# Performance work log

Hardware: AMD Instinct MI355X
Metric: run time of the kernel (lower is better)

The kernel has to match this reference:

```python
import jax, jax.numpy as jnp
import numpy as np

N_NODES = 20000
D = 512
H = 8
DK = D // H  # 64
L = 2


def _layernorm(x, g, b, eps=1e-5):
    mu = x.mean(-1, keepdims=True)
    var = x.var(-1, keepdims=True)
    return (x - mu) / jnp.sqrt(var + eps) * g + b


def _hgt_layer(h, kw, kb, qw, qb, vw, vb, aw, ab, pri, att_r, msg_r, skip, ln_g, ln_b, src, dst):
    # h: [N, D]
    N = h.shape[0]
    k = (h @ kw.T + kb).reshape(N, H, DK)
    q = (h @ qw.T + qb).reshape(N, H, DK)
    v = (h @ vw.T + vb).reshape(N, H, DK)
    # per-relation bilinear transforms on keys and messages
    k = jnp.einsum('nhi,hij->nhj', k, att_r)
    v = jnp.einsum('nhi,hij->nhj', v, msg_r)
    # per-edge attention scores [E, H]
    t = jnp.einsum('ehd,ehd->eh', k[src], q[dst]) * pri / jnp.sqrt(jnp.float32(DK))
    # edge softmax over incoming edges of each destination node
    mx = jax.ops.segment_max(t, dst, num_segments=N)
    e = jnp.exp(t - mx[dst])
    den = jax.ops.segment_sum(e, dst, num_segments=N)
    att = e / jnp.maximum(den[dst], 1e-9)
    # weighted message aggregation [N, H, DK] -> [N, D]
    msg = v[src] * att[..., None]
    agg = jax.ops.segment_sum(msg, dst, num_segments=N).reshape(N, D)
    trans = jax.nn.gelu(agg) @ aw.T + ab
    alpha = jax.nn.sigmoid(skip)
    out = trans * alpha + h * (1.0 - alpha)
    return _layernorm(out, ln_g, ln_b)


def setup_inputs() -> dict:
    key = jax.random.key(0)
    ks = jax.random.split(key, 16)
    B, E = 8192, 320000
    s = 0.02
    inp = {
        'embeddings': jax.random.normal(ks[0], (B, D), jnp.float32),
        'node_emb': jax.random.normal(ks[1], (N_NODES, D), jnp.float32) * s,
        'adapt_w': jax.random.normal(ks[2], (D, D), jnp.float32) * s,
        'adapt_b': jnp.zeros((D,), jnp.float32),
        'kw': jax.random.normal(ks[3], (L, D, D), jnp.float32) * s,
        'kb': jnp.zeros((L, D), jnp.float32),
        'qw': jax.random.normal(ks[4], (L, D, D), jnp.float32) * s,
        'qb': jnp.zeros((L, D), jnp.float32),
        'vw': jax.random.normal(ks[5], (L, D, D), jnp.float32) * s,
        'vb': jnp.zeros((L, D), jnp.float32),
        'aw': jax.random.normal(ks[6], (L, D, D), jnp.float32) * s,
        'ab': jnp.zeros((L, D), jnp.float32),
        'pri': jnp.ones((L, H), jnp.float32),
        'att_r': jax.random.normal(ks[7], (L, H, DK, DK), jnp.float32) * (1.0 / np.sqrt(DK)),
        'msg_r': jax.random.normal(ks[8], (L, H, DK, DK), jnp.float32) * (1.0 / np.sqrt(DK)),
        'skip': jnp.ones((L,), jnp.float32),
        'ln_g': jnp.ones((L, D), jnp.float32),
        'ln_b': jnp.zeros((L, D), jnp.float32),
        'out_w': jax.random.normal(ks[9], (D, D), jnp.float32) * s,
        'out_b': jnp.zeros((D,), jnp.float32),
        'attn_kernels': jax.random.uniform(ks[10], (D,), jnp.float32),
        'src': jax.random.randint(ks[11], (E,), 0, N_NODES, jnp.int32),
        'dst': jax.random.randint(ks[12], (E,), 0, N_NODES, jnp.int32),
        'n_classes': 10000,
    }
    return inp


def reference(embeddings, node_emb, adapt_w, adapt_b, kw, kb, qw, qb, vw, vb, aw, ab,
              pri, att_r, msg_r, skip, ln_g, ln_b, out_w, out_b, attn_kernels,
              src, dst, n_classes):
    # Hgt encoder over the label graph (single ntype '_N')
    h = jax.nn.gelu(node_emb @ adapt_w.T + adapt_b)
    for l in range(L):
        h = _hgt_layer(h, kw[l], kb[l], qw[l], qb[l], vw[l], vb[l], aw[l], ab[l],
                       pri[l], att_r[l], msg_r[l], skip[l], ln_g[l], ln_b[l], src, dst)
    cls_emb = h @ out_w.T + out_b          # [N, D]
    cls_emb = cls_emb[:n_classes]          # [C, D]  (dropout is identity in eval)
    # logits[b,c] = sum_d embeddings[b,d] * attn_kernels[d] * cls_emb[c,d]
    logits = (embeddings * attn_kernels) @ cls_emb.T
    return logits
```

## Files before the change

kernel.cpp:

```cpp
#include <hip/hip_runtime.h>
#include <hip/hip_bf16.h>

#define D 512
#define H 8
#define NLAYER 2

typedef __attribute__((ext_vector_type(8))) short short8;
typedef __attribute__((ext_vector_type(4))) short short4v;
typedef __attribute__((ext_vector_type(4))) float f32x4;

__device__ __forceinline__ float gelu_f(float x) {
    float x3 = x * x * x;
    return 0.5f * x * (1.0f + tanhf(0.7978845608028654f * (x + 0.044715f * x3)));
}

__device__ __forceinline__ unsigned short f2b(float x) {
    unsigned u = __float_as_uint(x);
    u += 0x7FFF + ((u >> 16) & 1);
    return (unsigned short)(u >> 16);
}
__device__ __forceinline__ float b2f(unsigned short u) {
    return __uint_as_float(((unsigned)u) << 16);
}

template <int POSTG, int OUTMODE>
__global__ __launch_bounds__(256) void gemm_bf(
    const short* __restrict__ A, const short* __restrict__ B,
    const float* __restrict__ bias, float* __restrict__ Cf,
    short* __restrict__ Cb, int M, int N, int K) {
    __shared__ __align__(16) short As[128 * 40];
    __shared__ __align__(16) short Bs[128 * 40];
    const unsigned gx = gridDim.x, gy = gridDim.y;
    const unsigned nwg = gx * gy;
    const unsigned orig = blockIdx.y * gx + blockIdx.x;
    const unsigned q = nwg >> 3, r = nwg & 7;
    const unsigned xcd = orig & 7, sidx = orig >> 3;
    const unsigned swz = (xcd < r ? xcd * (q + 1) : r * (q + 1) + (xcd - r) * q) + sidx;
    const unsigned CH = 8;
    const unsigned chunk = swz / (CH * gx);
    const unsigned rem = swz - chunk * (CH * gx);
    const unsigned nr = min(CH, gy - chunk * CH);
    const unsigned col = rem / nr;
    const unsigned rowin = rem - col * nr;
    const int bm = (int)(chunk * CH + rowin) * 128;
    const int bn = (int)col * 128;

    const int tid = threadIdx.x;
    const int lane = tid & 63;
    const int wave = tid >> 6;
    const int wm = (wave >> 1) * 64, wn = (wave & 1) * 64;
    const int lr16 = lane & 15;
    const int lk8 = (lane >> 4) * 8;

    const int srow = tid >> 1;
    const int skb = (tid & 1) * 16;
    const int arow = min(bm + srow, M - 1);
    const int brow = min(bn + srow, N - 1);
    const short* Ap = A + (size_t)arow * K + skb;
    const short* Bp = B + (size_t)brow * K + skb;

    f32x4 acc[4][4];
#pragma unroll
    for (int i = 0; i < 4; ++i)
#pragma unroll
        for (int j = 0; j < 4; ++j) acc[i][j] = (f32x4){0.f, 0.f, 0.f, 0.f};

    short8 ra0, ra1, rb0, rb1;
    auto load_ab = [&](int k0) {
        ra0 = *(const short8*)(Ap + k0);
        ra1 = *(const short8*)(Ap + k0 + 8);
        rb0 = *(const short8*)(Bp + k0);
        rb1 = *(const short8*)(Bp + k0 + 8);
    };

    load_ab(0);
    for (int k0 = 0; k0 < K; k0 += 32) {
        __syncthreads();
        *(short8*)&As[srow * 40 + skb]     = ra0;
        *(short8*)&As[srow * 40 + skb + 8] = ra1;
        *(short8*)&Bs[srow * 40 + skb]     = rb0;
        *(short8*)&Bs[srow * 40 + skb + 8] = rb1;
        __syncthreads();
        if (k0 + 32 < K) load_ab(k0 + 32);

        short8 af[4], bfr[4];
#pragma unroll
        for (int mi = 0; mi < 4; ++mi)
            af[mi] = *(const short8*)&As[(wm + mi * 16 + lr16) * 40 + lk8];
#pragma unroll
        for (int ni = 0; ni < 4; ++ni)
            bfr[ni] = *(const short8*)&Bs[(wn + ni * 16 + lr16) * 40 + lk8];
#pragma unroll
        for (int mi = 0; mi < 4; ++mi)
#pragma unroll
            for (int ni = 0; ni < 4; ++ni)
                acc[mi][ni] = __builtin_amdgcn_mfma_f32_16x16x32_bf16(
                    af[mi], bfr[ni], acc[mi][ni], 0, 0, 0);
    }

#pragma unroll
    for (int mi = 0; mi < 4; ++mi) {
        int row0 = bm + wm + mi * 16 + (lane >> 4) * 4;
#pragma unroll
        for (int ni = 0; ni < 4; ++ni) {
            int col2 = bn + wn + ni * 16 + lr16;
            if (col2 < N) {
                float bsv = bias ? bias[col2] : 0.0f;
#pragma unroll
                for (int rr2 = 0; rr2 < 4; ++rr2) {
                    int row = row0 + rr2;
                    if (row < M) {
                        float v = acc[mi][ni][rr2] + bsv;
                        if (POSTG) v = gelu_f(v);
                        if (OUTMODE != 1) Cf[(size_t)row * N + col2] = v;
                        if (OUTMODE != 0) Cb[(size_t)row * N + col2] = (short)f2b(v);
                    }
                }
            }
        }
    }
}

__global__ void cvt_b16(const float* __restrict__ in, short* __restrict__ out, int n8) {
    int i = blockIdx.x * 256 + threadIdx.x;
    if (i >= n8) return;
    float4 a = ((const float4*)in)[i * 2];
    float4 b = ((const float4*)in)[i * 2 + 1];
    short8 o;
    o[0] = f2b(a.x); o[1] = f2b(a.y); o[2] = f2b(a.z); o[3] = f2b(a.w);
    o[4] = f2b(b.x); o[5] = f2b(b.y); o[6] = f2b(b.z); o[7] = f2b(b.w);
    *(short8*)(out + (size_t)i * 8) = o;
}

__global__ void cp_f32(const float* __restrict__ in, float* __restrict__ out, int n) {
    int i = blockIdx.x * 256 + threadIdx.x;
    if (i < n) out[i] = in[i];
}

__global__ __launch_bounds__(256) void fuse_w(
    const float* __restrict__ w, const float* __restrict__ bsrc,
    const float* __restrict__ r, short* __restrict__ fw, float* __restrict__ fb) {
    int h = blockIdx.y;
    int dc = blockIdx.x * 64;
    __shared__ float rs[64][64];
    int tid = threadIdx.x;
    for (int i = tid; i < 4096; i += 256) rs[i >> 6][i & 63] = r[h * 4096 + i];
    __syncthreads();
    for (int rep = 0; rep < 16; ++rep) {
        int o = rep * 256 + tid;
        int j = o >> 6;
        int dd = o & 63;
        float s = 0.0f;
#pragma unroll 8
        for (int i = 0; i < 64; ++i)
            s = fmaf(rs[i][j], w[(size_t)(h * 64 + i) * D + dc + dd], s);
        fw[(size_t)(h * 64 + j) * D + dc + dd] = (short)f2b(s);
    }
    if (blockIdx.x == 0 && tid < 64) {
        float s = 0.0f;
        for (int i = 0; i < 64; ++i) s += bsrc[h * 64 + i] * rs[i][tid];
        fb[h * 64 + tid] = s;
    }
}

__global__ void zero_int(int* __restrict__ p, int n) {
    int i = blockIdx.x * 256 + threadIdx.x;
    if (i < n) p[i] = 0;
}

__global__ void hist_dst(const int* __restrict__ dst, int* __restrict__ cnt, int E) {
    int i = blockIdx.x * 256 + threadIdx.x;
    if (i < E) atomicAdd(&cnt[dst[i]], 1);
}

__global__ __launch_bounds__(1024) void scan_counts(
    const int* __restrict__ cnt, int* __restrict__ offs, int* __restrict__ cursor,
    int n, int E) {
    __shared__ int part[1024];
    int t = threadIdx.x;
    int chunk = (n + 1023) >> 10;
    int lo = t * chunk;
    int hi = min(lo + chunk, n);
    int s = 0;
    for (int i = lo; i < hi; ++i) s += cnt[i];
    part[t] = s;
    __syncthreads();
    for (int off = 1; off < 1024; off <<= 1) {
        int v = (t >= off) ? part[t - off] : 0;
        __syncthreads();
        part[t] += v;
        __syncthreads();
    }
    int base = (t == 0) ? 0 : part[t - 1];
    for (int i = lo; i < hi; ++i) {
        offs[i] = base;
        cursor[i] = base;
        base += cnt[i];
    }
    if (t == 1023) offs[n] = E;
}

__global__ void scatter_edges(const int* __restrict__ src, const int* __restrict__ dst,
                              int* __restrict__ cursor, int* __restrict__ srcs, int E) {
    int i = blockIdx.x * 256 + threadIdx.x;
    if (i < E) {
        int pos = atomicAdd(&cursor[dst[i]], 1);
        srcs[pos] = src[i];
    }
}

__global__ __launch_bounds__(256) void edge_attn(
    const short* __restrict__ kqv, const int* __restrict__ srcs,
    const int* __restrict__ offs, const float* __restrict__ pri,
    short* __restrict__ gg) {
    int n = blockIdx.x;
    int tid = threadIdx.x;
    int lane = tid & 63, wave = tid >> 6;
    int start = offs[n], end = offs[n + 1];

    __shared__ float t_lds[64][8];
    __shared__ float red[32][8];
    __shared__ float rm[8], rden[8], sc[8];
    __shared__ float part[4][512];

    const short8 qv = *(const short8*)(kqv + (size_t)n * 1536 + 512 + lane * 8);
    float qf[8];
#pragma unroll
    for (int j = 0; j < 8; ++j) qf[j] = b2f((unsigned short)qv[j]);
    const float prih = pri[lane >> 3] * 0.125f;

    if (tid < 8) { rm[tid] = -INFINITY; rden[tid] = 0.0f; }

    const int hh = lane >> 3;
    const int hr = tid & 7, sb = tid >> 3;
    float vacc[8];
#pragma unroll
    for (int j = 0; j < 8; ++j) vacc[j] = 0.0f;

    for (int base = start; base < end; base += 64) {
        int csz = min(64, end - base);
        __syncthreads();
        for (int s = wave; s < csz; s += 4) {
            int sn = srcs[base + s];
            short8 kv = *(const short8*)(kqv + (size_t)sn * 1536 + lane * 8);
            float sum = 0.0f;
#pragma unroll
            for (int j = 0; j < 8; ++j)
                sum = fmaf(b2f((unsigned short)kv[j]), qf[j], sum);
            sum += __shfl_xor(sum, 1);
            sum += __shfl_xor(sum, 2);
            sum += __shfl_xor(sum, 4);
            if ((lane & 7) == 0) t_lds[s][hh] = sum * prih;
        }
        __syncthreads();
        float m = -INFINITY;
        if (sb < csz) m = t_lds[sb][hr];
        if (sb + 32 < csz) m = fmaxf(m, t_lds[sb + 32][hr]);
        red[sb][hr] = m;
        __syncthreads();
        if (tid < 8) {
            float mm = -INFINITY;
#pragma unroll
            for (int s2 = 0; s2 < 32; ++s2) mm = fmaxf(mm, red[s2][tid]);
            float nm = fmaxf(rm[tid], mm);
            sc[tid] = expf(rm[tid] - nm);
            rm[tid] = nm;
        }
        __syncthreads();
        float m2 = rm[hh], scl = sc[hh];
#pragma unroll
        for (int j = 0; j < 8; ++j) vacc[j] *= scl;
        float mr = rm[hr];
        float se = 0.0f;
        if (sb < csz) se = expf(t_lds[sb][hr] - mr);
        if (sb + 32 < csz) se += expf(t_lds[sb + 32][hr] - mr);
        red[sb][hr] = se;
        __syncthreads();
        if (tid < 8) {
            float ssum = 0.0f;
#pragma unroll
            for (int s2 = 0; s2 < 32; ++s2) ssum += red[s2][tid];
            rden[tid] = rden[tid] * sc[tid] + ssum;
        }
        for (int s = wave; s < csz; s += 4) {
            int sn = srcs[base + s];
            float a = expf(t_lds[s][hh] - m2);
            short8 v = *(const short8*)(kqv + (size_t)sn * 1536 + 1024 + lane * 8);
#pragma unroll
            for (int j = 0; j < 8; ++j)
                vacc[j] = fmaf(b2f((unsigned short)v[j]), a, vacc[j]);
        }
    }
#pragma unroll
    for (int j = 0; j < 8; ++j) part[wave][lane * 8 + j] = vacc[j];
    __syncthreads();
    int c0 = tid * 2;
    float inv = 1.0f / fmaxf(rden[tid >> 5], 1e-9f);
    float s0 = (part[0][c0] + part[1][c0] + part[2][c0] + part[3][c0]) * inv;
    float s1 = (part[0][c0 + 1] + part[1][c0 + 1] + part[2][c0 + 1] + part[3][c0 + 1]) * inv;
    unsigned pack = (unsigned)(unsigned short)f2b(gelu_f(s0)) |
                    ((unsigned)(unsigned short)f2b(gelu_f(s1)) << 16);
    ((unsigned*)(gg + (size_t)n * D))[tid] = pack;
}

__global__ __launch_bounds__(128) void blend_ln(
    const float* __restrict__ trans, const float* __restrict__ hin,
    const float* __restrict__ skip, const float* __restrict__ g,
    const float* __restrict__ b, float* __restrict__ hout,
    short* __restrict__ hb16) {
    int n = blockIdx.x;
    int tid = threadIdx.x;
    float alpha = 1.0f / (1.0f + expf(-skip[0]));
    size_t base = (size_t)n * D + tid * 4;
    float4 t4 = *(const float4*)(trans + base);
    float4 h4 = *(const float4*)(hin + base);
    float o[4];
    o[0] = t4.x * alpha + h4.x * (1.0f - alpha);
    o[1] = t4.y * alpha + h4.y * (1.0f - alpha);
    o[2] = t4.z * alpha + h4.z * (1.0f - alpha);
    o[3] = t4.w * alpha + h4.w * (1.0f - alpha);
    float s = o[0] + o[1] + o[2] + o[3];
    float ss = o[0] * o[0] + o[1] * o[1] + o[2] * o[2] + o[3] * o[3];
    for (int off = 32; off; off >>= 1) {
        s += __shfl_down(s, off);
        ss += __shfl_down(ss, off);
    }
    __shared__ float red[4];
    if ((tid & 63) == 0) { red[tid >> 6] = s; red[2 + (tid >> 6)] = ss; }
    __syncthreads();
    float S = red[0] + red[1];
    float SS = red[2] + red[3];
    float mu = S * (1.0f / 512.0f);
    float var = SS * (1.0f / 512.0f) - mu * mu;
    float inv = rsqrtf(var + 1e-5f);
    int c = tid * 4;
    float4 o4;
    o4.x = (o[0] - mu) * inv * g[c + 0] + b[c + 0];
    o4.y = (o[1] - mu) * inv * g[c + 1] + b[c + 1];
    o4.z = (o[2] - mu) * inv * g[c + 2] + b[c + 2];
    o4.w = (o[3] - mu) * inv * g[c + 3] + b[c + 3];
    *(float4*)(hout + base) = o4;
    short4v hb;
    hb[0] = f2b(o4.x); hb[1] = f2b(o4.y); hb[2] = f2b(o4.z); hb[3] = f2b(o4.w);
    *(short4v*)(hb16 + base) = hb;
}

__global__ void scale_emb_b16(const float* __restrict__ e, const float* __restrict__ ak,
                              short* __restrict__ o, int n8) {
    int i = blockIdx.x * 256 + threadIdx.x;
    if (i >= n8) return;
    float4 a = ((const float4*)e)[i * 2];
    float4 b = ((const float4*)e)[i * 2 + 1];
    int d0 = (i * 8) & (D - 1);
    short8 v;
    v[0] = f2b(a.x * ak[d0 + 0]); v[1] = f2b(a.y * ak[d0 + 1]);
    v[2] = f2b(a.z * ak[d0 + 2]); v[3] = f2b(a.w * ak[d0 + 3]);
    v[4] = f2b(b.x * ak[d0 + 4]); v[5] = f2b(b.y * ak[d0 + 5]);
    v[6] = f2b(b.z * ak[d0 + 6]); v[7] = f2b(b.w * ak[d0 + 7]);
    *(short8*)(o + (size_t)i * 8) = v;
}

extern "C" void kernel_launch(void* const* d_in, const int* in_sizes, int n_in,
                              void* d_out, int out_size, void* d_ws, size_t ws_size,
                              hipStream_t stream) {
    const float* embeddings = (const float*)d_in[0];
    const float* node_emb   = (const float*)d_in[1];
    const float* adapt_w    = (const float*)d_in[2];
    const float* adapt_b    = (const float*)d_in[3];
    const float* kw   = (const float*)d_in[4];
    const float* kb   = (const float*)d_in[5];
    const float* qw   = (const float*)d_in[6];
    const float* qb   = (const float*)d_in[7];
    const float* vw   = (const float*)d_in[8];
    const float* vb   = (const float*)d_in[9];
    const float* aw   = (const float*)d_in[10];
    const float* ab   = (const float*)d_in[11];
    const float* pri  = (const float*)d_in[12];
    const float* att_r = (const float*)d_in[13];
    const float* msg_r = (const float*)d_in[14];
    const float* skip  = (const float*)d_in[15];
    const float* ln_g  = (const float*)d_in[16];
    const float* ln_b  = (const float*)d_in[17];
    const float* out_w = (const float*)d_in[18];
    const float* out_b = (const float*)d_in[19];
    const float* attn_k = (const float*)d_in[20];
    const int* src = (const int*)d_in[21];
    const int* dst = (const int*)d_in[22];

    const int E  = in_sizes[21];
    const int NB = in_sizes[0] / D;
    const int NN = in_sizes[1] / D;
    const int NC = out_size / NB;

    size_t big = (size_t)NN * D;
    float* hbuf = (float*)d_ws;
    float* fb32 = hbuf + big;
    short* hb16 = (short*)(fb32 + big);
    short* gg16 = hb16 + big;
    short* kqv16 = gg16 + big;
    short* w16a = kqv16 + (size_t)NN * 1536;
    short* w16o = w16a + (size_t)D * D;
    short* w16w = w16o + (size_t)D * D;
    short* wcat = w16w + (size_t)D * D;
    float* bcat = (float*)(wcat + (size_t)1536 * D);
    int* offs   = (int*)(bcat + 1536);
    int* cursor = offs + NN + 1;
    int* srcs   = cursor + NN;
    short* cls16 = kqv16;
    short* embs16 = kqv16 + (size_t)NC * D;

    auto ggrid = [](int M, int N) { return dim3((N + 127) / 128, (M + 127) / 128); };
    const int WB = D * D / 8;

    zero_int<<<(NN + 255) / 256, 256, 0, stream>>>(cursor, NN);
    hist_dst<<<(E + 255) / 256, 256, 0, stream>>>(dst, cursor, E);
    scan_counts<<<1, 1024, 0, stream>>>(cursor, offs, cursor, NN, E);
    scatter_edges<<<(E + 255) / 256, 256, 0, stream>>>(src, dst, cursor, srcs, E);

    cvt_b16<<<((int)(big / 8) + 255) / 256, 256, 0, stream>>>(node_emb, gg16, (int)(big / 8));
    cvt_b16<<<(WB + 255) / 256, 256, 0, stream>>>(adapt_w, w16a, WB);
    cvt_b16<<<(WB + 255) / 256, 256, 0, stream>>>(out_w, w16o, WB);

    gemm_bf<1, 2><<<ggrid(NN, D), 256, 0, stream>>>(gg16, w16a, adapt_b, hbuf, hb16, NN, D, D);

    for (int l = 0; l < NLAYER; ++l) {
        const size_t wo = (size_t)l * D * D;
        fuse_w<<<dim3(8, 8), 256, 0, stream>>>(kw + wo, kb + l * D, att_r + (size_t)l * H * 64 * 64, wcat, bcat);
        cvt_b16<<<(WB + 255) / 256, 256, 0, stream>>>(qw + wo, wcat + (size_t)512 * D, WB);
        cp_f32<<<2, 256, 0, stream>>>(qb + l * D, bcat + 512, D);
        fuse_w<<<dim3(8, 8), 256, 0, stream>>>(vw + wo, vb + l * D, msg_r + (size_t)l * H * 64 * 64, wcat + (size_t)1024 * D, bcat + 1024);

        gemm_bf<0, 1><<<ggrid(NN, 1536), 256, 0, stream>>>(hb16, wcat, bcat, nullptr, kqv16, NN, 1536, D);

        edge_attn<<<NN, 256, 0, stream>>>(kqv16, srcs, offs, pri + l * H, gg16);

        cvt_b16<<<(WB + 255) / 256, 256, 0, stream>>>(aw + wo, w16w, WB);
        gemm_bf<0, 0><<<ggrid(NN, D), 256, 0, stream>>>(gg16, w16w, ab + l * D, fb32, nullptr, NN, D, D);
        blend_ln<<<NN, 128, 0, stream>>>(fb32, hbuf, skip + l, ln_g + l * D, ln_b + l * D, hbuf, hb16);
    }

    gemm_bf<0, 1><<<ggrid(NC, D), 256, 0, stream>>>(hb16, w16o, out_b, nullptr, cls16, NC, D, D);
    scale_emb_b16<<<((NB * D / 8) + 255) / 256, 256, 0, stream>>>(embeddings, attn_k, embs16, NB * D / 8);
    gemm_bf<0, 0><<<ggrid(NB, NC), 256, 0, stream>>>(embs16, cls16, nullptr, (float*)d_out, nullptr, NB, NC, D);
}
```

Before: 880.9 us.

## Use one wave per node with online softmax and double GEMM K-tile

The edge attention kernel now gives each destination node a single wave instead of a whole 256-thread block. It computes a per-edge online softmax in registers, which removes the shared-memory reductions and the many block barriers for each chunk of edges. Separately, the bf16 GEMM K tile grows from 32 to 64, with the LDS stride changed to match, so barriers are halved and more MFMAs run per sync. The cost is a serial edge loop per wave with no parallelism across edges, plus larger LDS use per block in the GEMM.

```diff
diff --git a/kernel.cpp b/kernel.cpp
--- a/kernel.cpp
+++ b/kernel.cpp
@@ -28,8 +28,8 @@
     const short* __restrict__ A, const short* __restrict__ B,
     const float* __restrict__ bias, float* __restrict__ Cf,
     short* __restrict__ Cb, int M, int N, int K) {
-    __shared__ __align__(16) short As[128 * 40];
-    __shared__ __align__(16) short Bs[128 * 40];
+    __shared__ __align__(16) short As[128 * 72];
+    __shared__ __align__(16) short Bs[128 * 72];
     const unsigned gx = gridDim.x, gy = gridDim.y;
     const unsigned nwg = gx * gy;
     const unsigned orig = blockIdx.y * gx + blockIdx.x;
@@ -53,7 +53,7 @@
     const int lk8 = (lane >> 4) * 8;
 
     const int srow = tid >> 1;
-    const int skb = (tid & 1) * 16;
+    const int skb = (tid & 1) * 32;
     const int arow = min(bm + srow, M - 1);
     const int brow = min(bn + srow, N - 1);
     const short* Ap = A + (size_t)arow * K + skb;
@@ -65,37 +65,42 @@
 #pragma unroll
         for (int j = 0; j < 4; ++j) acc[i][j] = (f32x4){0.f, 0.f, 0.f, 0.f};
 
-    short8 ra0, ra1, rb0, rb1;
+    short8 ra[4], rb[4];
     auto load_ab = [&](int k0) {
-        ra0 = *(const short8*)(Ap + k0);
-        ra1 = *(const short8*)(Ap + k0 + 8);
-        rb0 = *(const short8*)(Bp + k0);
-        rb1 = *(const short8*)(Bp + k0 + 8);
+#pragma unroll
+        for (int u = 0; u < 4; ++u) {
+            ra[u] = *(const short8*)(Ap + k0 + u * 8);
+            rb[u] = *(const short8*)(Bp + k0 + u * 8);
+        }
     };
 
     load_ab(0);
-    for (int k0 = 0; k0 < K; k0 += 32) {
+    for (int k0 = 0; k0 < K; k0 += 64) {
         __syncthreads();
-        *(short8*)&As[srow * 40 + skb]     = ra0;
-        *(short8*)&As[srow * 40 + skb + 8] = ra1;
-        *(short8*)&Bs[srow * 40 + skb]     = rb0;
-        *(short8*)&Bs[srow * 40 + skb + 8] = rb1;
+#pragma unroll
+        for (int u = 0; u < 4; ++u) {
+            *(short8*)&As[srow * 72 + skb + u * 8] = ra[u];
+            *(short8*)&Bs[srow * 72 + skb + u * 8] = rb[u];
+        }
         __syncthreads();
-        if (k0 + 32 < K) load_ab(k0 + 32);
-
-        short8 af[4], bfr[4];
-#pragma unroll
-        for (int mi = 0; mi < 4; ++mi)
-            af[mi] = *(const short8*)&As[(wm + mi * 16 + lr16) * 40 + lk8];
-#pragma unroll
-        for (int ni = 0; ni < 4; ++ni)
-            bfr[ni] = *(const short8*)&Bs[(wn + ni * 16 + lr16) * 40 + lk8];
-#pragma unroll
-        for (int mi = 0; mi < 4; ++mi)
+        if (k0 + 64 < K) load_ab(k0 + 64);
+
+#pragma unroll
+        for (int kk = 0; kk < 2; ++kk) {
+            short8 af[4], bfr[4];
+#pragma unroll
+            for (int mi = 0; mi < 4; ++mi)
+                af[mi] = *(const short8*)&As[(wm + mi * 16 + lr16) * 72 + kk * 32 + lk8];
 #pragma unroll
             for (int ni = 0; ni < 4; ++ni)
-                acc[mi][ni] = __builtin_amdgcn_mfma_f32_16x16x32_bf16(
-                    af[mi], bfr[ni], acc[mi][ni], 0, 0, 0);
+                bfr[ni] = *(const short8*)&Bs[(wn + ni * 16 + lr16) * 72 + kk * 32 + lk8];
+#pragma unroll
+            for (int mi = 0; mi < 4; ++mi)
+#pragma unroll
+                for (int ni = 0; ni < 4; ++ni)
+                    acc[mi][ni] = __builtin_amdgcn_mfma_f32_16x16x32_bf16(
+                        af[mi], bfr[ni], acc[mi][ni], 0, 0, 0);
+        }
     }
 
 #pragma unroll
@@ -212,16 +217,11 @@
 __global__ __launch_bounds__(256) void edge_attn(
     const short* __restrict__ kqv, const int* __restrict__ srcs,
     const int* __restrict__ offs, const float* __restrict__ pri,
-    short* __restrict__ gg) {
-    int n = blockIdx.x;
-    int tid = threadIdx.x;
-    int lane = tid & 63, wave = tid >> 6;
+    short* __restrict__ gg, int NNodes) {
+    int n = blockIdx.x * 4 + (threadIdx.x >> 6);
+    if (n >= NNodes) return;
+    int lane = threadIdx.x & 63;
     int start = offs[n], end = offs[n + 1];
-
-    __shared__ float t_lds[64][8];
-    __shared__ float red[32][8];
-    __shared__ float rm[8], rden[8], sc[8];
-    __shared__ float part[4][512];
 
     const short8 qv = *(const short8*)(kqv + (size_t)n * 1536 + 512 + lane * 8);
     float qf[8];
@@ -229,78 +229,45 @@
     for (int j = 0; j < 8; ++j) qf[j] = b2f((unsigned short)qv[j]);
     const float prih = pri[lane >> 3] * 0.125f;
 
-    if (tid < 8) { rm[tid] = -INFINITY; rden[tid] = 0.0f; }
-
-    const int hh = lane >> 3;
-    const int hr = tid & 7, sb = tid >> 3;
+    float rm = -INFINITY, rden = 0.0f;
     float vacc[8];
 #pragma unroll
     for (int j = 0; j < 8; ++j) vacc[j] = 0.0f;
 
-    for (int base = start; base < end; base += 64) {
-        int csz = min(64, end - base);
-        __syncthreads();
-        for (int s = wave; s < csz; s += 4) {
-            int sn = srcs[base + s];
-            short8 kv = *(const short8*)(kqv + (size_t)sn * 1536 + lane * 8);
-            float sum = 0.0f;
-#pragma unroll
-            for (int j = 0; j < 8; ++j)
-                sum = fmaf(b2f((unsigned short)kv[j]), qf[j], sum);
-            sum += __shfl_xor(sum, 1);
-            sum += __shfl_xor(sum, 2);
-            sum += __shfl_xor(sum, 4);
-            if ((lane & 7) == 0) t_lds[s][hh] = sum * prih;
-        }
-        __syncthreads();
-        float m = -INFINITY;
-        if (sb < csz) m = t_lds[sb][hr];
-        if (sb + 32 < csz) m = fmaxf(m, t_lds[sb + 32][hr]);
-        red[sb][hr] = m;
-        __syncthreads();
-        if (tid < 8) {
-            float mm = -INFINITY;
-#pragma unroll
-            for (int s2 = 0; s2 < 32; ++s2) mm = fmaxf(mm, red[s2][tid]);
-            float nm = fmaxf(rm[tid], mm);
-            sc[tid] = expf(rm[tid] - nm);
-            rm[tid] = nm;
-        }
-        __syncthreads();
-        float m2 = rm[hh], scl = sc[hh];
-#pragma unroll
-        for (int j = 0; j < 8; ++j) vacc[j] *= scl;
-        float mr = rm[hr];
-        float se = 0.0f;
-        if (sb < csz) se = expf(t_lds[sb][hr] - mr);
-        if (sb + 32 < csz) se += expf(t_lds[sb + 32][hr] - mr);
-        red[sb][hr] = se;
-        __syncthreads();
-        if (tid < 8) {
-            float ssum = 0.0f;
-#pragma unroll
-            for (int s2 = 0; s2 < 32; ++s2) ssum += red[s2][tid];
-            rden[tid] = rden[tid] * sc[tid] + ssum;
-        }
-        for (int s = wave; s < csz; s += 4) {
-            int sn = srcs[base + s];
-            float a = expf(t_lds[s][hh] - m2);
-            short8 v = *(const short8*)(kqv + (size_t)sn * 1536 + 1024 + lane * 8);
-#pragma unroll
-            for (int j = 0; j < 8; ++j)
-                vacc[j] = fmaf(b2f((unsigned short)v[j]), a, vacc[j]);
-        }
-    }
-#pragma unroll
-    for (int j = 0; j < 8; ++j) part[wave][lane * 8 + j] = vacc[j];
-    __syncthreads();
-    int c0 = tid * 2;
-    float inv = 1.0f / fmaxf(rden[tid >> 5], 1e-9f);
-    float s0 = (part[0][c0] + part[1][c0] + part[2][c0] + part[3][c0]) * inv;
-    float s1 = (part[0][c0 + 1] + part[1][c0 + 1] + part[2][c0 + 1] + part[3][c0 + 1]) * inv;
-    unsigned pack = (unsigned)(unsigned short)f2b(gelu_f(s0)) |
-                    ((unsigned)(unsigned short)f2b(gelu_f(s1)) << 16);
-    ((unsigned*)(gg + (size_t)n * D))[tid] = pack;
+    for (int i = start; i < end; ++i) {
+        int sn = srcs[i];
+        const short* row = kqv + (size_t)sn * 1536;
+        short8 kv = *(const short8*)(row + lane * 8);
+        short8 vv = *(const short8*)(row + 1024 + lane * 8);
+        float sum = 0.0f;
+#pragma unroll
+        for (int j = 0; j < 8; ++j)
+            sum = fmaf(b2f((unsigned short)kv[j]), qf[j], sum);
+        sum += __shfl_xor(sum, 1);
+        sum += __shfl_xor(sum, 2);
+        sum += __shfl_xor(sum, 4);
+        float tt = sum * prih;
+        float nm = fmaxf(rm, tt);
+        float scl = expf(rm - nm);
+        float e = expf(tt - nm);
+        rden = rden * scl + e;
+        rm = nm;
+#pragma unroll
+        for (int j = 0; j < 8; ++j)
+            vacc[j] = fmaf(vacc[j], scl, b2f((unsigned short)vv[j]) * e);
+    }
+
+    float inv = 1.0f / fmaxf(rden, 1e-9f);
+    unsigned o[4];
+#pragma unroll
+    for (int p = 0; p < 4; ++p) {
+        float s0 = gelu_f(vacc[2 * p] * inv);
+        float s1 = gelu_f(vacc[2 * p + 1] * inv);
+        o[p] = (unsigned)(unsigned short)f2b(s0) |
+               ((unsigned)(unsigned short)f2b(s1) << 16);
+    }
+    uint4 pack = make_uint4(o[0], o[1], o[2], o[3]);
+    *(uint4*)(gg + (size_t)n * D + lane * 8) = pack;
 }
 
 __global__ __launch_bounds__(128) void blend_ln(
@@ -432,7 +399,7 @@
 
         gemm_bf<0, 1><<<ggrid(NN, 1536), 256, 0, stream>>>(hb16, wcat, bcat, nullptr, kqv16, NN, 1536, D);
 
-        edge_attn<<<NN, 256, 0, stream>>>(kqv16, srcs, offs, pri + l * H, gg16);
+        edge_attn<<<(NN + 3) / 4, 256, 0, stream>>>(kqv16, srcs, offs, pri + l * H, gg16, NN);
 
         cvt_b16<<<(WB + 255) / 256, 256, 0, stream>>>(aw + wo, w16w, WB);
         gemm_bf<0, 0><<<ggrid(NN, D), 256, 0, stream>>>(gg16, w16w, ab + l * D, fb32, nullptr, NN, D, D);
```

Result: no change. 875.1 us (-0.7%).
